# Kernel optimization log

Hardware: AMD Instinct MI355X
Metric: run time of the kernel (lower is better)

The kernel has to match this reference:

```python
import jax, jax.numpy as jnp
import numpy as np

N, K, D = 65536, 1024, 256
COMMIT = 0.25
EPS = 1e-12


def setup_inputs() -> dict:
    key = jax.random.key(0)
    kx, kw = jax.random.split(key)
    x = jax.random.normal(kx, (N, D), dtype=jnp.float32)
    # nn.Embedding weight init: uniform(-1/vector_num, 1/vector_num)
    weight = jax.random.uniform(kw, (K, D), dtype=jnp.float32,
                                minval=-1.0 / K, maxval=1.0 / K)
    return {"x": x, "weight": weight}


def reference(x, weight):
    distances = (jnp.sum(x * x, axis=1, keepdims=True)
                 + jnp.sum(weight * weight, axis=1)
                 - 2.0 * (x @ weight.T))
    vector_indices = jnp.argmin(distances, axis=1)              # [N]
    quantized = weight[vector_indices]                          # gather == one-hot @ weight

    e_latent_loss = jnp.mean((jax.lax.stop_gradient(quantized) - x) ** 2)
    q_latent_loss = jnp.mean((quantized - jax.lax.stop_gradient(x)) ** 2)
    quant_loss = q_latent_loss + COMMIT * e_latent_loss

    # straight-through estimator
    quantized_out = x + jax.lax.stop_gradient(quantized - x)

    # utilization: counts of each code (== column sums of one-hot encodings)
    counts = jnp.zeros((K,), x.dtype).at[vector_indices].add(1.0)
    util_loss = jnp.mean(jnp.abs(counts - x.shape[0] / K))

    # compactness: 2 * mean of pairwise euclidean distances among codebook rows
    sq = jnp.sum(weight * weight, axis=1)
    pd2 = sq[:, None] + sq[None, :] - 2.0 * (weight @ weight.T)  # [K, K]
    iu = jnp.triu(jnp.ones((K, K), bool), 1)
    pd = jnp.sqrt(jnp.maximum(jnp.where(iu, pd2, 1.0), EPS))
    n_pairs = K * (K - 1) // 2
    compact_loss = 2.0 * jnp.sum(jnp.where(iu, pd, 0.0)) / n_pairs

    return quantized_out, quant_loss, util_loss, compact_loss, vector_indices
```

## Files before the change

kernel.cpp:

```cpp
#include <hip/hip_runtime.h>
#include <math.h>

#define NROWS 65536
#define KCODES 1024
#define DDIM 256
#define ND_TOT (NROWS * DDIM)

#define WS_IDX      0
#define WS_COUNTS   262144
#define WS_SW       266240
#define WS_PARTQ    532480
#define WS_PARTP    536576
#define WS_FLAGCNT  540672
#define WS_FLAGLIST 540928
#define WS_WH       803072
#define WS_WL       1327360

typedef float f32x4 __attribute__((ext_vector_type(4)));
typedef short bf16x8 __attribute__((ext_vector_type(8)));

__device__ inline unsigned short f2bf(float f) {
  unsigned u = __float_as_uint(f);
  u += 0x7FFFu + ((u >> 16) & 1u);
  return (unsigned short)(u >> 16);
}
__device__ inline float bf2f(unsigned short h) {
  return __uint_as_float(((unsigned)h) << 16);
}

__device__ inline void gload16(const void* g, void* l) {
  __builtin_amdgcn_global_load_lds((const __attribute__((address_space(1))) void*)g,
                                   (__attribute__((address_space(3))) void*)l, 16, 0, 0);
}

__global__ __launch_bounds__(256) void vq_prep(const float* __restrict__ x,
                                               const float* __restrict__ w,
                                               unsigned short* __restrict__ xh,
                                               unsigned short* __restrict__ xl,
                                               float* __restrict__ sw,
                                               unsigned short* __restrict__ wh,
                                               unsigned short* __restrict__ wl,
                                               int* __restrict__ counts,
                                               int* __restrict__ flagCnt) {
#pragma clang fp contract(off)
  const int b = blockIdx.x;
  const int t = threadIdx.x;
  if (b >= 2048) {
    const int lane = t & 63, wv = t >> 6;
    const int row = (b - 2048) * 4 + wv;
    const float* src = w + (size_t)row * DDIM;
    float4 v4 = *(const float4*)&src[lane * 4];
    float fv[4] = {v4.x, v4.y, v4.z, v4.w};
    union { unsigned short us[4]; uint2 v; } ph, pl;
#pragma unroll
    for (int e = 0; e < 4; ++e) {
      unsigned short h = f2bf(fv[e]);
      ph.us[e] = h;
      pl.us[e] = f2bf(fv[e] - bf2f(h));
    }
    *(uint2*)&wh[(size_t)row * DDIM + lane * 4] = ph.v;
    *(uint2*)&wl[(size_t)row * DDIM + lane * 4] = pl.v;
    float acc = 0.f;
    if (lane < 16) {
      const float* p = src + ((lane >> 3) & 1) * 128 + (lane & 7);
      float v = p[0];
      acc = v * v;
      for (int k = 1; k < 16; ++k) { float vv = p[k * 8]; float e = vv * vv; acc = acc + e; }
    }
    acc = acc + __shfl_xor(acc, 1);
    acc = acc + __shfl_xor(acc, 2);
    acc = acc + __shfl_xor(acc, 4);
    const float hb = __shfl(acc, 8);
    if (lane == 0) sw[row] = acc + hb;
    return;
  }
  if (b == 0) {
#pragma unroll
    for (int j = 0; j < 4; ++j) counts[j * 256 + t] = 0;
    if (t == 0) flagCnt[0] = 0;
  }
  const size_t tid = (size_t)b * 256 + t;
  float4 a[4], c[4];
#pragma unroll
  for (int g = 0; g < 4; ++g) {
    const size_t e = ((size_t)g * 524288 + tid) * 8;
    a[g] = *(const float4*)&x[e];
    c[g] = *(const float4*)&x[e + 4];
  }
#pragma unroll
  for (int g = 0; g < 4; ++g) {
    const size_t e = ((size_t)g * 524288 + tid) * 8;
    float fv[8] = {a[g].x, a[g].y, a[g].z, a[g].w, c[g].x, c[g].y, c[g].z, c[g].w};
    union { unsigned short us[8]; uint4 v; } ph, pl;
#pragma unroll
    for (int k = 0; k < 8; ++k) {
      unsigned short h = f2bf(fv[k]);
      ph.us[k] = h;
      pl.us[k] = f2bf(fv[k] - bf2f(h));
    }
    *(uint4*)&xh[e] = ph.v;
    *(uint4*)&xl[e] = pl.v;
  }
}

#define TRM 128
#define BKM 64
#define REPAIR_T 1.5e-4f

__global__ __launch_bounds__(256, 2) void vq_argmin_mfma(
    const unsigned short* __restrict__ xh, const unsigned short* __restrict__ xl,
    const unsigned short* __restrict__ wh, const unsigned short* __restrict__ wl,
    const float* __restrict__ sw,
    int* __restrict__ idxOut, float* __restrict__ idxOutF,
    int* __restrict__ flagCnt, int* __restrict__ flagList) {
  __shared__ __align__(16) unsigned short lds_xh[TRM * BKM];
  __shared__ __align__(16) unsigned short lds_xl[TRM * BKM];
  __shared__ __align__(16) unsigned short lds_wh[TRM * BKM];
  __shared__ __align__(16) unsigned short lds_wl[TRM * BKM];
  __shared__ __align__(16) float sws[KCODES];
  __shared__ float mrgB1[TRM][2];
  __shared__ float mrgB2[TRM][2];
  __shared__ int   mrgI[TRM][2];

  const int t = threadIdx.x;
  const int lane = t & 63, wv = t >> 6;
  const int wr = wv >> 1, wc = wv & 1;
  const int row0 = blockIdx.x * TRM;

  { f32x4 v = ((const f32x4*)sw)[t]; ((f32x4*)sws)[t] = v; }

  const int laneRow = lane >> 3;
  const int srcswz = ((lane & 7) * 16) ^ ((laneRow & 7) << 4);
  const char* xhB = (const char*)xh;
  const char* xlB = (const char*)xl;
  const char* whB = (const char*)wh;
  const char* wlB = (const char*)wl;

  float b1[16], b2[16];
  int bi[16];
#pragma unroll
  for (int s = 0; s < 16; ++s) { b1[s] = 3.4e38f; b2[s] = 3.4e38f; bi[s] = 0; }

  for (int ct = 0; ct < KCODES / TRM; ++ct) {
    f32x4 acc[4][4];
#pragma unroll
    for (int i = 0; i < 4; ++i)
#pragma unroll
      for (int j = 0; j < 4; ++j) acc[i][j] = (f32x4){0.f, 0.f, 0.f, 0.f};

    for (int dt = 0; dt < 4; ++dt) {
      __syncthreads();
#pragma unroll
      for (int i = 0; i < 4; ++i) {
        const int rb = wv * 32 + i * 8;
        const size_t gox = (size_t)(row0 + rb + laneRow) * 512 + (size_t)(dt * 128 + srcswz);
        gload16(xhB + gox, (char*)lds_xh + rb * 128);
        gload16(xlB + gox, (char*)lds_xl + rb * 128);
        const size_t gow = (size_t)(ct * 128 + rb + laneRow) * 512 + (size_t)(dt * 128 + srcswz);
        gload16(whB + gow, (char*)lds_wh + rb * 128);
        gload16(wlB + gow, (char*)lds_wl + rb * 128);
      }
      __syncthreads();

#pragma unroll
      for (int kh = 0; kh < 2; ++kh) {
        const int kb = kh * 64 + (lane >> 4) * 16;
        bf16x8 ah[4], al[4];
#pragma unroll
        for (int i = 0; i < 4; ++i) {
          const int r = wr * 64 + i * 16 + (lane & 15);
          const int off = r * 128 + (kb ^ ((r & 7) << 4));
          ah[i] = *(const bf16x8*)((const char*)lds_xh + off);
          al[i] = *(const bf16x8*)((const char*)lds_xl + off);
        }
#pragma unroll
        for (int j = 0; j < 4; ++j) {
          const int c = wc * 64 + j * 16 + (lane & 15);
          const int off = c * 128 + (kb ^ ((c & 7) << 4));
          bf16x8 bh = *(const bf16x8*)((const char*)lds_wh + off);
          bf16x8 bl = *(const bf16x8*)((const char*)lds_wl + off);
#pragma unroll
          for (int i = 0; i < 4; ++i) {
            acc[i][j] = __builtin_amdgcn_mfma_f32_16x16x32_bf16(ah[i], bh, acc[i][j], 0, 0, 0);
            acc[i][j] = __builtin_amdgcn_mfma_f32_16x16x32_bf16(ah[i], bl, acc[i][j], 0, 0, 0);
            acc[i][j] = __builtin_amdgcn_mfma_f32_16x16x32_bf16(al[i], bh, acc[i][j], 0, 0, 0);
          }
        }
      }
    }

#pragma unroll
    for (int j = 0; j < 4; ++j) {
      const int colbase = ct * 128 + wc * 64 + j * 16 + (lane & 15);
      const float swv = sws[colbase];
#pragma unroll
      for (int i = 0; i < 4; ++i)
#pragma unroll
        for (int q = 0; q < 4; ++q) {
          const int s = i * 4 + q;
          const float e = fmaf(-2.f, acc[i][j][q], swv);
          const bool c1 = e < b1[s];
          b2[s] = c1 ? b1[s] : fminf(b2[s], e);
          bi[s] = c1 ? colbase : bi[s];
          b1[s] = fminf(b1[s], e);
        }
    }
  }

#pragma unroll
  for (int off = 1; off < 16; off <<= 1) {
#pragma unroll
    for (int s = 0; s < 16; ++s) {
      const float ob1 = __shfl_xor(b1[s], off);
      const float ob2 = __shfl_xor(b2[s], off);
      const int oi = __shfl_xor(bi[s], off);
      const float hi = fmaxf(b1[s], ob1);
      const bool take = ob1 < b1[s];
      b1[s] = fminf(b1[s], ob1);
      b2[s] = fminf(hi, fminf(b2[s], ob2));
      bi[s] = take ? oi : bi[s];
    }
  }
  if ((lane & 15) == 0) {
#pragma unroll
    for (int i = 0; i < 4; ++i)
#pragma unroll
      for (int q = 0; q < 4; ++q) {
        const int s = i * 4 + q;
        const int r = wr * 64 + i * 16 + (lane >> 4) * 4 + q;
        mrgB1[r][wc] = b1[s]; mrgB2[r][wc] = b2[s]; mrgI[r][wc] = bi[s];
      }
  }
  __syncthreads();
  if (t < TRM) {
    const float b1a = mrgB1[t][0], b1b = mrgB1[t][1];
    const float b2a = mrgB2[t][0], b2b = mrgB2[t][1];
    const bool take = b1b < b1a;
    const float b1f = fminf(b1a, b1b);
    const float b2f = fminf(fmaxf(b1a, b1b), fminf(b2a, b2b));
    const int idxf = take ? mrgI[t][1] : mrgI[t][0];
    const int grow = row0 + t;
    idxOut[grow] = idxf;
    idxOutF[grow] = (float)idxf;
    const bool flag = (b2f - b1f) < REPAIR_T;
    unsigned long long m = __ballot(flag);
    int base2 = 0;
    if ((t & 63) == 0) base2 = atomicAdd(flagCnt, __popcll(m));
    base2 = __shfl(base2, 0);
    if (flag) flagList[base2 + __popcll(m & ((1ull << (t & 63)) - 1ull))] = grow;
  }
}

#define RPB 8
__global__ __launch_bounds__(256) void vq_repair_compact(
    const float* __restrict__ x, const float* __restrict__ w,
    const float* __restrict__ sw,
    const int* __restrict__ flagCnt, const int* __restrict__ flagList,
    int* __restrict__ idxOut, float* __restrict__ idxOutF,
    float* __restrict__ partialP) {
  const int t = threadIdx.x;
  if (blockIdx.x >= 1024) {
    const int i = blockIdx.x - 1024;
    __shared__ float wi[DDIM];
    wi[t] = w[(size_t)i * DDIM + t];
    __syncthreads();
    float swi = sw[i];
    double s = 0.0;
    for (int j = i + 1 + t; j < KCODES; j += 256) {
      const float4* wj = (const float4*)(w + (size_t)j * DDIM);
      const float4* wi4 = (const float4*)wi;
      float acc = 0.f;
#pragma unroll 8
      for (int d4 = 0; d4 < DDIM / 4; ++d4) {
        float4 a = wi4[d4];
        float4 b = wj[d4];
        acc += a.x * b.x + a.y * b.y + a.z * b.z + a.w * b.w;
      }
      float pd2 = (swi + sw[j]) - 2.0f * acc;
      s += (double)sqrtf(fmaxf(pd2, 1e-12f));
    }
    for (int off = 32; off > 0; off >>= 1) s += __shfl_down(s, off);
    __shared__ double redc[4];
    if ((t & 63) == 0) redc[t >> 6] = s;
    __syncthreads();
    if (t == 0)
      partialP[i] = (float)(redc[0] + redc[1] + redc[2] + redc[3]);
    return;
  }
  __shared__ float xrow[RPB][DDIM];
  __shared__ float sxsh[RPB];
  __shared__ float rd[RPB][256];
  __shared__ int ri[RPB][256];
  const int cnt = flagCnt[0];
  for (int base = blockIdx.x * RPB; base < cnt; base += 1024 * RPB) {
    const int nr = min(RPB, cnt - base);
    int rowIdx[RPB];
#pragma unroll
    for (int r = 0; r < RPB; ++r)
      rowIdx[r] = flagList[base + ((r < nr) ? r : 0)];
    __syncthreads();
    for (int r = 0; r < nr; ++r)
      xrow[r][t] = x[(size_t)rowIdx[r] * DDIM + t];
    __syncthreads();
    if (t < nr) {
#pragma clang fp contract(off)
      float halves[2];
#pragma unroll
      for (int h = 0; h < 2; ++h) {
        const float* p = &xrow[t][h * 128];
        float acc[8];
#pragma unroll
        for (int j = 0; j < 8; ++j) { float v = p[j]; acc[j] = v * v; }
        for (int i = 8; i < 128; i += 8) {
#pragma unroll
          for (int j = 0; j < 8; ++j) { float v = p[i + j]; float e = v * v; acc[j] = acc[j] + e; }
        }
        halves[h] = ((acc[0] + acc[1]) + (acc[2] + acc[3])) + ((acc[4] + acc[5]) + (acc[6] + acc[7]));
      }
      sxsh[t] = halves[0] + halves[1];
    }
    __syncthreads();
    float bD[RPB]; int bI[RPB];
#pragma unroll
    for (int r = 0; r < RPB; ++r) { bD[r] = 3.4e38f; bI[r] = 0x7fffffff; }
    for (int g = 0; g < 4; ++g) {
      const int c = g * 256 + t;
      const float4* wrp = (const float4*)(w + (size_t)c * DDIM);
      float acc[RPB];
#pragma unroll
      for (int r = 0; r < RPB; ++r) acc[r] = 0.f;
      for (int d4 = 0; d4 < DDIM / 4; ++d4) {
        const float4 wv = wrp[d4];
#pragma unroll
        for (int e = 0; e < 4; ++e) {
          const float wvx = (e == 0) ? wv.x : (e == 1) ? wv.y : (e == 2) ? wv.z : wv.w;
#pragma unroll
          for (int r = 0; r < RPB; ++r) acc[r] = fmaf(xrow[r][d4 * 4 + e], wvx, acc[r]);
        }
      }
      const float swc = sw[c];
#pragma unroll
      for (int r = 0; r < RPB; ++r) {
        const float tt = sxsh[r] + swc;
        const float dist = tt - 2.0f * acc[r];
        if (dist < bD[r]) { bD[r] = dist; bI[r] = c; }
      }
    }
#pragma unroll
    for (int r = 0; r < RPB; ++r) { rd[r][t] = bD[r]; ri[r][t] = bI[r]; }
    __syncthreads();
    for (int s2 = 128; s2 > 0; s2 >>= 1) {
      if (t < s2) {
#pragma unroll
        for (int r = 0; r < RPB; ++r) {
          const float od = rd[r][t + s2]; const int oi = ri[r][t + s2];
          if (od < rd[r][t] || (od == rd[r][t] && oi < ri[r][t])) { rd[r][t] = od; ri[r][t] = oi; }
        }
      }
      __syncthreads();
    }
    if (t < nr) {
      const int row = rowIdx[t];
      idxOut[row] = ri[t][0];
      idxOutF[row] = (float)ri[t][0];
    }
    __syncthreads();
  }
}

__global__ __launch_bounds__(256) void vq_quantize(const float* __restrict__ x,
                                                   const float* __restrict__ w,
                                                   const int* __restrict__ idxArr,
                                                   float* __restrict__ qout,
                                                   int* __restrict__ counts,
                                                   float* __restrict__ partialQ) {
  const int wave = threadIdx.x >> 6;
  const int lane = threadIdx.x & 63;
  const int base = blockIdx.x * 64 + wave * 16;
  float s = 0.f;
#pragma unroll 4
  for (int r = 0; r < 16; ++r) {
    const int row = base + r;
    const int idx = idxArr[row];
    float4 xv = ((const float4*)(x + (size_t)row * DDIM))[lane];
    float4 qv = ((const float4*)(w + (size_t)idx * DDIM))[lane];
    float dx = qv.x - xv.x, dy = qv.y - xv.y, dz = qv.z - xv.z, dw = qv.w - xv.w;
    float4 o;
    o.x = xv.x + dx; o.y = xv.y + dy; o.z = xv.z + dz; o.w = xv.w + dw;
    ((float4*)(qout + (size_t)row * DDIM))[lane] = o;
    s += dx * dx + dy * dy + dz * dz + dw * dw;
    if (lane == 0) atomicAdd(&counts[idx], 1);
  }
  double d = s;
  for (int off = 32; off > 0; off >>= 1) d += __shfl_down(d, off);
  __shared__ double red[4];
  if (lane == 0) red[wave] = d;
  __syncthreads();
  if (threadIdx.x == 0)
    partialQ[blockIdx.x] = (float)(red[0] + red[1] + red[2] + red[3]);
}

__global__ __launch_bounds__(1024) void vq_final(const float* __restrict__ partialQ,
                                                 const float* __restrict__ partialP,
                                                 const int* __restrict__ counts,
                                                 float* __restrict__ out) {
  const int t = threadIdx.x;
  const int lane = t & 63, wave = t >> 6;
  double q = (double)partialQ[t];
  double p = (double)partialP[t];
  double u = (double)fabsf((float)counts[t] - 64.0f);
  for (int off = 32; off > 0; off >>= 1) {
    q += __shfl_down(q, off);
    p += __shfl_down(p, off);
    u += __shfl_down(u, off);
  }
  __shared__ double redQ[16], redP[16], redU[16];
  if (lane == 0) { redQ[wave] = q; redP[wave] = p; redU[wave] = u; }
  __syncthreads();
  if (t == 0) {
    double sq = 0, sp = 0, su = 0;
    for (int j = 0; j < 16; ++j) { sq += redQ[j]; sp += redP[j]; su += redU[j]; }
    float m = (float)(sq / 16777216.0);
    out[ND_TOT] = m + 0.25f * m;
    out[ND_TOT + 1] = (float)(su / 1024.0);
    out[ND_TOT + 2] = (float)(2.0 * sp / 523776.0);
  }
}

extern "C" void kernel_launch(void* const* d_in, const int* in_sizes, int n_in,
                              void* d_out, int out_size, void* d_ws, size_t ws_size,
                              hipStream_t stream) {
  const float* x = (const float*)d_in[0];
  const float* w = (const float*)d_in[1];
  float* out = (float*)d_out;

  char* ws = (char*)d_ws;
  int* wsIdx    = (int*)(ws + WS_IDX);
  int* counts   = (int*)(ws + WS_COUNTS);
  float* swv    = (float*)(ws + WS_SW);
  float* partQ  = (float*)(ws + WS_PARTQ);
  float* partP  = (float*)(ws + WS_PARTP);
  int* flagCnt  = (int*)(ws + WS_FLAGCNT);
  int* flagList = (int*)(ws + WS_FLAGLIST);
  unsigned short* whS = (unsigned short*)(ws + WS_WH);
  unsigned short* wlS = (unsigned short*)(ws + WS_WL);

  unsigned short* xhS = (unsigned short*)d_out;
  unsigned short* xlS = xhS + (size_t)ND_TOT;

  vq_prep<<<2304, 256, 0, stream>>>(x, w, xhS, xlS, swv, whS, wlS, counts, flagCnt);
  vq_argmin_mfma<<<NROWS / TRM, 256, 0, stream>>>(xhS, xlS, whS, wlS, swv,
                                                  wsIdx, out + ND_TOT + 3, flagCnt, flagList);
  vq_repair_compact<<<2048, 256, 0, stream>>>(x, w, swv, flagCnt, flagList,
                                              wsIdx, out + ND_TOT + 3, partP);
  vq_quantize<<<1024, 256, 0, stream>>>(x, w, wsIdx, out, counts, partQ);
  vq_final<<<1, 1024, 0, stream>>>(partQ, partP, counts, out);
}
```

Baseline: 264.8 us.

## Move codebook compactness blocks into prep kernel and batch quantize loads

The pairwise codebook-distance blocks move from the repair kernel into the prep kernel. They recompute each row norm locally, so they no longer depend on the sw array written by prep, and the work overlaps with the conversion blocks. The repair kernel now handles only flagged rows, with rows per block raised from 8 to 16. The quantize loop issues four rows of index, x and codebook loads before computing, to raise memory-level parallelism. The cost is extra redundant norm arithmetic, because each row norm is recomputed for every pair, plus larger shared-memory use in repair, which may lower occupancy.

```diff
diff --git a/kernel.cpp b/kernel.cpp
--- a/kernel.cpp
+++ b/kernel.cpp
@@ -41,11 +41,46 @@
                                                unsigned short* __restrict__ wh,
                                                unsigned short* __restrict__ wl,
                                                int* __restrict__ counts,
-                                               int* __restrict__ flagCnt) {
-#pragma clang fp contract(off)
+                                               int* __restrict__ flagCnt,
+                                               float* __restrict__ partialP) {
   const int b = blockIdx.x;
   const int t = threadIdx.x;
+  if (b >= 2304) {
+    const int i = b - 2304;
+    const int lane = t & 63, wv = t >> 6;
+    __shared__ float wi[DDIM];
+    __shared__ float redw[4];
+    __shared__ double redc[4];
+    float v = w[(size_t)i * DDIM + t];
+    wi[t] = v;
+    float sq = v * v;
+    for (int off = 32; off; off >>= 1) sq += __shfl_down(sq, off);
+    if (lane == 0) redw[wv] = sq;
+    __syncthreads();
+    const float swi = redw[0] + redw[1] + redw[2] + redw[3];
+    double s = 0.0;
+    for (int j = i + 1 + t; j < KCODES; j += 256) {
+      const float4* wj = (const float4*)(w + (size_t)j * DDIM);
+      const float4* wi4 = (const float4*)wi;
+      float accd = 0.f, accs = 0.f;
+#pragma unroll 8
+      for (int d4 = 0; d4 < DDIM / 4; ++d4) {
+        float4 a = wi4[d4];
+        float4 bv = wj[d4];
+        accd += a.x * bv.x + a.y * bv.y + a.z * bv.z + a.w * bv.w;
+        accs += bv.x * bv.x + bv.y * bv.y + bv.z * bv.z + bv.w * bv.w;
+      }
+      float pd2 = (swi + accs) - 2.0f * accd;
+      s += (double)sqrtf(fmaxf(pd2, 1e-12f));
+    }
+    for (int off = 32; off; off >>= 1) s += __shfl_down(s, off);
+    if (lane == 0) redc[wv] = s;
+    __syncthreads();
+    if (t == 0) partialP[i] = (float)(redc[0] + redc[1] + redc[2] + redc[3]);
+    return;
+  }
   if (b >= 2048) {
+#pragma clang fp contract(off)
     const int lane = t & 63, wv = t >> 6;
     const int row = (b - 2048) * 4 + wv;
     const float* src = w + (size_t)row * DDIM;
@@ -251,46 +286,19 @@
   }
 }
 
-#define RPB 8
-__global__ __launch_bounds__(256) void vq_repair_compact(
-    const float* __restrict__ x, const float* __restrict__ w,
-    const float* __restrict__ sw,
-    const int* __restrict__ flagCnt, const int* __restrict__ flagList,
-    int* __restrict__ idxOut, float* __restrict__ idxOutF,
-    float* __restrict__ partialP) {
-  const int t = threadIdx.x;
-  if (blockIdx.x >= 1024) {
-    const int i = blockIdx.x - 1024;
-    __shared__ float wi[DDIM];
-    wi[t] = w[(size_t)i * DDIM + t];
-    __syncthreads();
-    float swi = sw[i];
-    double s = 0.0;
-    for (int j = i + 1 + t; j < KCODES; j += 256) {
-      const float4* wj = (const float4*)(w + (size_t)j * DDIM);
-      const float4* wi4 = (const float4*)wi;
-      float acc = 0.f;
-#pragma unroll 8
-      for (int d4 = 0; d4 < DDIM / 4; ++d4) {
-        float4 a = wi4[d4];
-        float4 b = wj[d4];
-        acc += a.x * b.x + a.y * b.y + a.z * b.z + a.w * b.w;
-      }
-      float pd2 = (swi + sw[j]) - 2.0f * acc;
-      s += (double)sqrtf(fmaxf(pd2, 1e-12f));
-    }
-    for (int off = 32; off > 0; off >>= 1) s += __shfl_down(s, off);
-    __shared__ double redc[4];
-    if ((t & 63) == 0) redc[t >> 6] = s;
-    __syncthreads();
-    if (t == 0)
-      partialP[i] = (float)(redc[0] + redc[1] + redc[2] + redc[3]);
-    return;
-  }
+#define RPB 16
+__global__ __launch_bounds__(256) void vq_repair(const float* __restrict__ x,
+                                                 const float* __restrict__ w,
+                                                 const float* __restrict__ sw,
+                                                 const int* __restrict__ flagCnt,
+                                                 const int* __restrict__ flagList,
+                                                 int* __restrict__ idxOut,
+                                                 float* __restrict__ idxOutF) {
   __shared__ float xrow[RPB][DDIM];
   __shared__ float sxsh[RPB];
   __shared__ float rd[RPB][256];
   __shared__ int ri[RPB][256];
+  const int t = threadIdx.x;
   const int cnt = flagCnt[0];
   for (int base = blockIdx.x * RPB; base < cnt; base += 1024 * RPB) {
     const int nr = min(RPB, cnt - base);
@@ -378,18 +386,28 @@
   const int lane = threadIdx.x & 63;
   const int base = blockIdx.x * 64 + wave * 16;
   float s = 0.f;
-#pragma unroll 4
-  for (int r = 0; r < 16; ++r) {
-    const int row = base + r;
-    const int idx = idxArr[row];
-    float4 xv = ((const float4*)(x + (size_t)row * DDIM))[lane];
-    float4 qv = ((const float4*)(w + (size_t)idx * DDIM))[lane];
-    float dx = qv.x - xv.x, dy = qv.y - xv.y, dz = qv.z - xv.z, dw = qv.w - xv.w;
-    float4 o;
-    o.x = xv.x + dx; o.y = xv.y + dy; o.z = xv.z + dz; o.w = xv.w + dw;
-    ((float4*)(qout + (size_t)row * DDIM))[lane] = o;
-    s += dx * dx + dy * dy + dz * dz + dw * dw;
-    if (lane == 0) atomicAdd(&counts[idx], 1);
+#pragma unroll
+  for (int rg = 0; rg < 4; ++rg) {
+    int idx4[4];
+#pragma unroll
+    for (int r = 0; r < 4; ++r) idx4[r] = idxArr[base + rg * 4 + r];
+    float4 xv[4], qv[4];
+#pragma unroll
+    for (int r = 0; r < 4; ++r) {
+      xv[r] = ((const float4*)(x + (size_t)(base + rg * 4 + r) * DDIM))[lane];
+      qv[r] = ((const float4*)(w + (size_t)idx4[r] * DDIM))[lane];
+    }
+#pragma unroll
+    for (int r = 0; r < 4; ++r) {
+      const int row = base + rg * 4 + r;
+      float dx = qv[r].x - xv[r].x, dy = qv[r].y - xv[r].y;
+      float dz = qv[r].z - xv[r].z, dw = qv[r].w - xv[r].w;
+      float4 o;
+      o.x = xv[r].x + dx; o.y = xv[r].y + dy; o.z = xv[r].z + dz; o.w = xv[r].w + dw;
+      ((float4*)(qout + (size_t)row * DDIM))[lane] = o;
+      s += dx * dx + dy * dy + dz * dz + dw * dw;
+      if (lane == 0) atomicAdd(&counts[idx4[r]], 1);
+    }
   }
   double d = s;
   for (int off = 32; off > 0; off >>= 1) d += __shfl_down(d, off);
@@ -448,11 +466,10 @@
   unsigned short* xhS = (unsigned short*)d_out;
   unsigned short* xlS = xhS + (size_t)ND_TOT;
 
-  vq_prep<<<2304, 256, 0, stream>>>(x, w, xhS, xlS, swv, whS, wlS, counts, flagCnt);
+  vq_prep<<<3328, 256, 0, stream>>>(x, w, xhS, xlS, swv, whS, wlS, counts, flagCnt, partP);
   vq_argmin_mfma<<<NROWS / TRM, 256, 0, stream>>>(xhS, xlS, whS, wlS, swv,
                                                   wsIdx, out + ND_TOT + 3, flagCnt, flagList);
-  vq_repair_compact<<<2048, 256, 0, stream>>>(x, w, swv, flagCnt, flagList,
-                                              wsIdx, out + ND_TOT + 3, partP);
+  vq_repair<<<1024, 256, 0, stream>>>(x, w, swv, flagCnt, flagList, wsIdx, out + ND_TOT + 3);
   vq_quantize<<<1024, 256, 0, stream>>>(x, w, wsIdx, out, counts, partQ);
   vq_final<<<1, 1024, 0, stream>>>(partQ, partP, counts, out);
 }
```

New measurement: 384.4 us. +45.2%, slower.
